# Performance work log

Hardware: AMD Instinct MI355X
Metric: run time of the kernel (lower is better)

## Reference

```python
import jax, jax.numpy as jnp
import numpy as np


def setup_inputs() -> dict:
    key = jax.random.key(0)
    k1, k2, k3, k4 = jax.random.split(key, 4)
    B, Tv, Ta, D = 8, 2048, 2048, 256
    return {
        "visual_features": jax.random.normal(k1, (B, Tv, D), dtype=jnp.float32),
        "audio_features": jax.random.normal(k2, (B, Ta, D), dtype=jnp.float32),
        "visual_weights": jax.random.uniform(k3, (D, D), dtype=jnp.float32),
        "audio_weights": jax.random.uniform(k4, (D, D), dtype=jnp.float32),
        "num_neighbors": 8,
    }


def _pairwise_l2(vm, am):
    # ||v - a|| via the expanded form to avoid the [B,Tv,Ta,D] intermediate.
    sq = (
        jnp.sum(vm * vm, -1)[:, :, None]
        + jnp.sum(am * am, -1)[:, None, :]
        - 2.0 * jnp.einsum("btd,bsd->bts", vm, am)
    )
    sq = jnp.maximum(sq, 0.0)
    # safe sqrt: subgradient 0 at 0 (matches torch.norm backward convention)
    return jnp.where(sq > 0, jnp.sqrt(jnp.where(sq > 0, sq, 1.0)), 0.0)


def reference(visual_features, audio_features, visual_weights, audio_weights, num_neighbors):
    vm = visual_features @ visual_weights  # [B,Tv,D]
    am = audio_features @ audio_weights    # [B,Ta,D]
    graph = jnp.exp(-_pairwise_l2(vm, am))  # [B,Tv,Ta]
    # topk over the visual axis (dim=1): move it last for lax.top_k
    _, idx = jax.lax.top_k(jnp.swapaxes(graph, 1, 2), num_neighbors)  # [B,Ta,k]
    idx = jnp.swapaxes(idx, 1, 2)  # [B,k,Ta]
    # broadcasted gather along axis 1: result [B,k,Ta,D]
    vn = jnp.take_along_axis(visual_features[:, :, None, :], idx[..., None], axis=1)
    an = jnp.take_along_axis(audio_features[:, :, None, :], idx[..., None], axis=1)
    # mean over dim=2 (the Ta axis of the gathered neighbors) -> [B,k,D]
    return vn.mean(axis=2), an.mean(axis=2)
```

## Files before the change

### kernel.cpp

```cpp
#include <hip/hip_runtime.h>
#include <cstddef>
#include <cstdint>

namespace {
constexpr int kB   = 8;
constexpr int kT   = 2048;
constexpr int kD   = 256;
constexpr int kK   = 8;
constexpr int kM   = kB * kT;
constexpr int kNCH = 64;
constexpr int kNC  = kB * kT;
constexpr int kColCap = 64;
constexpr int kOvCap  = 1 << 17;
constexpr int kStr = 264;
constexpr float kMinNormalF = 1.17549435e-38f;
}

typedef __attribute__((ext_vector_type(8)))  __bf16 bf16x8;
typedef __attribute__((ext_vector_type(16))) float  f32x16;

__device__ inline unsigned short f2bf_rne(float x) {
  unsigned u = __float_as_uint(x);
  unsigned r = (u + 0x7FFFu + ((u >> 16) & 1u)) >> 16;
  return (unsigned short)r;
}
__device__ inline float bf2f(unsigned short h) {
  return __uint_as_float((unsigned)h << 16);
}
union FragU { uint4 u4; bf16x8 v; };

__global__ __launch_bounds__(256) void transposeW2(const float* __restrict__ W0,
                                                   const float* __restrict__ W1,
                                                   unsigned short* __restrict__ T0,
                                                   unsigned short* __restrict__ T1) {
  const float* W = blockIdx.z ? W1 : W0;
  unsigned short* WT = blockIdx.z ? T1 : T0;
  __shared__ float tile[32][33];
  const int k0 = blockIdx.y * 32, c0 = blockIdx.x * 32;
  const int tx = threadIdx.x & 31, ty = threadIdx.x >> 5;
#pragma unroll
  for (int i = 0; i < 4; ++i)
    tile[ty + i * 8][tx] = W[(size_t)(k0 + ty + i * 8) * kD + c0 + tx];
  __syncthreads();
#pragma unroll
  for (int i = 0; i < 4; ++i)
    WT[(size_t)(c0 + ty + i * 8) * kD + k0 + tx] = f2bf_rne(tile[tx][ty + i * 8]);
}

__global__ __launch_bounds__(256) void gemm_hyb(const float* __restrict__ Xv,
                                                const float* __restrict__ Xa,
                                                const unsigned short* __restrict__ WvT,
                                                const unsigned short* __restrict__ WaT,
                                                unsigned short* __restrict__ Cv,
                                                unsigned short* __restrict__ Ca,
                                                float* __restrict__ nv,
                                                float* __restrict__ na) {
  __shared__ unsigned short S[64 * kStr];
  const int z = blockIdx.y;
  const float* X = z ? Xa : Xv;
  const unsigned short* WT = z ? WaT : WvT;
  unsigned short* Cb = z ? Ca : Cv;
  float* nrm = z ? na : nv;
  const int r0 = blockIdx.x * 64;
  const int tid = threadIdx.x;
  const int w = tid >> 6, lane = tid & 63;
  const int wt = w & 1, wc = w >> 1;
  const int half = lane >> 5, ln = lane & 31;

#pragma unroll
  for (int i = 0; i < 16; ++i) {
    const int idx = i * 256 + tid;
    const int row = idx >> 6, g = idx & 63;
    const float4 v = *reinterpret_cast<const float4*>(X + (size_t)(r0 + row) * kD + g * 4);
    ushort4 o;
    o.x = f2bf_rne(v.x); o.y = f2bf_rne(v.y); o.z = f2bf_rne(v.z); o.w = f2bf_rne(v.w);
    *reinterpret_cast<ushort4*>(S + row * kStr + g * 4) = o;
  }
  __syncthreads();
  uint4 afr[16];
#pragma unroll
  for (int kc = 0; kc < 16; ++kc)
    afr[kc] = *reinterpret_cast<const uint4*>(S + (wt * 32 + ln) * kStr + kc * 16 + half * 8);

  float ns[16];
#pragma unroll
  for (int r = 0; r < 16; ++r) ns[r] = 0.0f;

  for (int ct = 0; ct < 4; ++ct) {
    const int c0 = ct * 64;
    __syncthreads();
#pragma unroll
    for (int i = 0; i < 8; ++i) {
      const int idx = i * 256 + tid;
      const int row = idx >> 5, g = idx & 31;
      const uint4 v = *reinterpret_cast<const uint4*>(WT + (size_t)(c0 + row) * kD + g * 8);
      *reinterpret_cast<uint4*>(S + row * kStr + g * 8) = v;
    }
    __syncthreads();
    f32x16 acc;
#pragma unroll
    for (int i = 0; i < 16; ++i) acc[i] = 0.0f;
#pragma unroll
    for (int kc = 0; kc < 16; ++kc) {
      FragU fa, fb;
      fa.u4 = afr[kc];
      fb.u4 = *reinterpret_cast<const uint4*>(S + (wc * 32 + ln) * kStr + kc * 16 + half * 8);
      acc = __builtin_amdgcn_mfma_f32_32x32x16_bf16(fa.v, fb.v, acc, 0, 0, 0);
    }
    const int col = c0 + wc * 32 + ln;
#pragma unroll
    for (int r = 0; r < 16; ++r) {
      const int row = r0 + wt * 32 + (r & 3) + 8 * (r >> 2) + 4 * half;
      const unsigned short us = f2bf_rne(acc[r]);
      Cb[(size_t)row * kD + col] = us;
      const float f = bf2f(us);
      ns[r] += f * f;
    }
  }
#pragma unroll
  for (int r = 0; r < 16; ++r) {
    float v = ns[r];
#pragma unroll
    for (int off = 1; off < 32; off <<= 1) v += __shfl_xor(v, off, 64);
    if (ln == 0) {
      const int row = r0 + wt * 32 + (r & 3) + 8 * (r >> 2) + 4 * half;
      atomicAdd(nrm + row, v);
    }
  }
}

__global__ __launch_bounds__(256) void keys_hyb(const unsigned short* __restrict__ vmb,
                                                const unsigned short* __restrict__ amb,
                                                const float* __restrict__ vn2,
                                                const float* __restrict__ an2,
                                                unsigned* __restrict__ colCount,
                                                uint2* __restrict__ colRecs,
                                                unsigned* __restrict__ ovCount,
                                                uint2* __restrict__ ovRecs) {
  __shared__ unsigned short S[64 * kStr];
  const int b = blockIdx.z;
  const int t0 = blockIdx.x * 64;
  const int sr0 = blockIdx.y * 128;
  const int tid = threadIdx.x;
  const int w = tid >> 6, lane = tid & 63;
  const int wt = w & 1, wsc = w >> 1;
  const int half = lane >> 5, ln = lane & 31;

#pragma unroll
  for (int i = 0; i < 8; ++i) {
    const int idx = i * 256 + tid;
    const int row = idx >> 5, g = idx & 31;
    const uint4 v = *reinterpret_cast<const uint4*>(vmb + ((size_t)b * kT + t0 + row) * kD + g * 8);
    *reinterpret_cast<uint4*>(S + row * kStr + g * 8) = v;
  }
  __syncthreads();
  uint4 afr[16];
#pragma unroll
  for (int kc = 0; kc < 16; ++kc)
    afr[kc] = *reinterpret_cast<const uint4*>(S + (wt * 32 + ln) * kStr + kc * 16 + half * 8);

  const float* v2p = vn2 + (size_t)b * kT + t0 + wt * 32;

  for (int st = 0; st < 2; ++st) {
    const int s0 = sr0 + st * 64;
    __syncthreads();
#pragma unroll
    for (int i = 0; i < 8; ++i) {
      const int idx = i * 256 + tid;
      const int row = idx >> 5, g = idx & 31;
      const uint4 v = *reinterpret_cast<const uint4*>(amb + ((size_t)b * kT + s0 + row) * kD + g * 8);
      *reinterpret_cast<uint4*>(S + row * kStr + g * 8) = v;
    }
    __syncthreads();
    f32x16 acc;
#pragma unroll
    for (int i = 0; i < 16; ++i) acc[i] = 0.0f;
#pragma unroll
    for (int kc = 0; kc < 16; ++kc) {
      FragU fa, fb;
      fa.u4 = afr[kc];
      fb.u4 = *reinterpret_cast<const uint4*>(S + (wsc * 32 + ln) * kStr + kc * 16 + half * 8);
      acc = __builtin_amdgcn_mfma_f32_32x32x16_bf16(fa.v, fb.v, acc, 0, 0, 0);
    }
    const int s = s0 + wsc * 32 + ln;
    const float a2 = an2[(size_t)b * kT + s];
    const int c = (b << 11) | s;
#pragma unroll
    for (int g = 0; g < 4; ++g) {
      const float4 v2 = *reinterpret_cast<const float4*>(v2p + g * 8 + half * 4);
      const float v2a[4] = {v2.x, v2.y, v2.z, v2.w};
#pragma unroll
      for (int q = 0; q < 4; ++q) {
        const float raw = v2a[q] + a2 - 2.0f * acc[4 * g + q];
        if (raw < 7744.0f) {
          const float dist = sqrtf(fmaxf(raw, 0.0f));
          const float e = expf(-dist);
          if (e >= kMinNormalF) {
            const int t = t0 + wt * 32 + g * 8 + half * 4 + q;
            const unsigned slot = atomicAdd(&colCount[c], 1u);
            if (slot < (unsigned)kColCap) {
              colRecs[(size_t)c * kColCap + slot] = make_uint2(__float_as_uint(e), (unsigned)t);
            } else {
              const unsigned pos = ((unsigned)b << 22) | ((unsigned)s << 11) | (unsigned)t;
              const unsigned oi = atomicAdd(ovCount, 1u);
              if (oi < (unsigned)kOvCap) ovRecs[oi] = make_uint2(__float_as_uint(e), pos);
            }
          }
        }
      }
    }
  }
}

__global__ __launch_bounds__(256) void finalize_topk(const unsigned* __restrict__ colCount,
                                                     const uint2* __restrict__ colRecs,
                                                     const unsigned* __restrict__ ovCount,
                                                     const uint2* __restrict__ ovRecs,
                                                     int* __restrict__ idxT) {
  const int c = blockIdx.x * 256 + threadIdx.x;
  unsigned K[8];
  int T[8];
#pragma unroll
  for (int i = 0; i < 8; ++i) { K[i] = 0u; T[i] = 0x7FFFFFFF; }
  const int cnt = (int)colCount[c];
  const int m = min(cnt, kColCap);
  for (int i = 0; i < m; ++i) {
    const uint2 r = colRecs[(size_t)c * kColCap + i];
    const unsigned kx = r.x;
    const int tx = (int)r.y;
    if (kx > K[7] || (kx == K[7] && tx < T[7])) {
      K[7] = kx; T[7] = tx;
#pragma unroll
      for (int q = 7; q >= 1; --q) {
        const bool sw = (K[q] > K[q - 1]) || (K[q] == K[q - 1] && T[q] < T[q - 1]);
        if (sw) {
          const unsigned tk = K[q]; K[q] = K[q - 1]; K[q - 1] = tk;
          const int tt = T[q];      T[q] = T[q - 1]; T[q - 1] = tt;
        }
      }
    }
  }
  if (cnt > kColCap) {
    int n = (int)*ovCount;
    if (n > kOvCap) n = kOvCap;
    for (int i = 0; i < n; ++i) {
      const uint2 r = ovRecs[i];
      if ((int)(r.y >> 11) == c) {
        const unsigned kx = r.x;
        const int tx = (int)(r.y & 2047u);
        if (kx > K[7] || (kx == K[7] && tx < T[7])) {
          K[7] = kx; T[7] = tx;
#pragma unroll
          for (int q = 7; q >= 1; --q) {
            const bool sw = (K[q] > K[q - 1]) || (K[q] == K[q - 1] && T[q] < T[q - 1]);
            if (sw) {
              const unsigned tk = K[q]; K[q] = K[q - 1]; K[q - 1] = tk;
              const int tt = T[q];      T[q] = T[q - 1]; T[q - 1] = tt;
            }
          }
        }
      }
    }
  }
  int mcnt = 0;
#pragma unroll
  for (int i = 0; i < 8; ++i) if (K[i] > 0u) mcnt++;
  int outv[8];
#pragma unroll
  for (int i = 0; i < 8; ++i) outv[i] = T[i];
  int cand = 0;
  for (int r = mcnt; r < 8; ++r) {
    bool taken = true;
    while (taken) {
      taken = false;
#pragma unroll
      for (int q = 0; q < 8; ++q)
        if (q < mcnt && T[q] == cand) taken = true;
      if (taken) cand++;
    }
    outv[r] = cand++;
  }
  const int b = c >> 11, s = c & 2047;
#pragma unroll
  for (int r = 0; r < 8; ++r) idxT[((size_t)b * kK + r) * kT + s] = outv[r];
}

__global__ __launch_bounds__(256) void gather_kernel(const float* __restrict__ visual,
                                                     const float* __restrict__ audio,
                                                     const int* __restrict__ idxT,
                                                     float* __restrict__ pv,
                                                     float* __restrict__ pa) {
  const int blk = blockIdx.x;
  const int ch = blk & (kNCH - 1);
  const int bj = blk / kNCH;
  const int b = bj >> 3;
  const int d = threadIdx.x;
  const int* ip = idxT + (size_t)bj * kT + ch * (kT / kNCH);
  float accV = 0.f, accA = 0.f;
  for (int g = 0; g < kT / kNCH / 4; ++g) {
    const int4 cur = *reinterpret_cast<const int4*>(ip + g * 4);
    const int ts[4] = {cur.x, cur.y, cur.z, cur.w};
#pragma unroll
    for (int u = 0; u < 4; ++u) {
      const size_t base = ((size_t)b * kT + ts[u]) * kD + d;
      accV += visual[base];
      accA += audio[base];
    }
  }
  pv[(size_t)blk * kD + d] = accV;
  pa[(size_t)blk * kD + d] = accA;
}

__global__ __launch_bounds__(256) void reduce_kernel(const float* __restrict__ pv,
                                                     const float* __restrict__ pa,
                                                     float* __restrict__ out) {
  const int bj = blockIdx.x;
  const int d = threadIdx.x;
  float sV = 0.f, sA = 0.f;
#pragma unroll 8
  for (int ch = 0; ch < kNCH; ++ch) {
    sV += pv[((size_t)bj * kNCH + ch) * kD + d];
    sA += pa[((size_t)bj * kNCH + ch) * kD + d];
  }
  out[(size_t)bj * kD + d] = sV * (1.0f / kT);
  out[(size_t)kB * kK * kD + (size_t)bj * kD + d] = sA * (1.0f / kT);
}

extern "C" void kernel_launch(void* const* d_in, const int* in_sizes, int n_in,
                              void* d_out, int out_size, void* d_ws, size_t ws_size,
                              hipStream_t stream) {
  (void)in_sizes; (void)n_in; (void)out_size; (void)ws_size;
  const float* visual = (const float*)d_in[0];
  const float* audio  = (const float*)d_in[1];
  const float* Wv     = (const float*)d_in[2];
  const float* Wa     = (const float*)d_in[3];
  float* out = (float*)d_out;

  char* ws = (char*)d_ws;
  unsigned short* WvT = (unsigned short*)ws;
  unsigned short* WaT = WvT + (size_t)kD * kD;
  unsigned short* vmb = WaT + (size_t)kD * kD;
  unsigned short* amb = vmb + (size_t)kM * kD;
  float* vn2 = (float*)(amb + (size_t)kM * kD);
  float* an2 = vn2 + kM;
  unsigned* colCount = (unsigned*)(an2 + kM);
  unsigned* ovCount  = colCount + kNC;
  uint2* colRecs = (uint2*)(ovCount + 4);
  uint2* ovRecs  = colRecs + (size_t)kNC * kColCap;
  int* idxT = (int*)(ovRecs + kOvCap);
  float* pv = (float*)(idxT + (size_t)kB * kK * kT);
  float* pa = pv + (size_t)kB * kK * kNCH * kD;

  hipMemsetAsync(vn2, 0, (size_t)(2 * kM + kNC + 4) * sizeof(float), stream);
  transposeW2<<<dim3(kD / 32, kD / 32, 2), 256, 0, stream>>>(Wv, Wa, WvT, WaT);
  gemm_hyb<<<dim3(kM / 64, 2), 256, 0, stream>>>(visual, audio, WvT, WaT,
                                                 vmb, amb, vn2, an2);
  keys_hyb<<<dim3(kT / 64, kT / 128, kB), 256, 0, stream>>>(vmb, amb, vn2, an2,
                                                            colCount, colRecs, ovCount, ovRecs);
  finalize_topk<<<dim3(kNC / 256), 256, 0, stream>>>(colCount, colRecs, ovCount, ovRecs, idxT);
  gather_kernel<<<dim3(kB * kK * kNCH), 256, 0, stream>>>(visual, audio, idxT, pv, pa);
  reduce_kernel<<<dim3(kB * kK), 256, 0, stream>>>(pv, pa, out);
}
```

Measured before the change: 179.4 us.

## Enlarge distance-kernel tiles, split projection GEMM columns, fuse memset into prep

The pairwise-distance kernel now gives each block 128 visual rows by 256 audio rows, with each wave owning 32 visual rows and computing two 32x32 MFMA tiles per audio sub-tile. This raises reuse of the A fragments held in registers and cuts how often audio tiles are reloaded from global memory. The projection GEMM is split over two column halves to double block count. The workspace memset is folded into the weight-transpose kernel to remove a launch. The trade-offs are more accumulator registers per wave and fewer blocks in the distance kernel, while the GEMM split converts the X tile twice and adds atomic norm updates.

Measured after the change: 175.5 us. -2.2%, faster.

```diff
diff --git a/kernel.cpp b/kernel.cpp
--- a/kernel.cpp
+++ b/kernel.cpp
@@ -29,22 +29,31 @@
 }
 union FragU { uint4 u4; bf16x8 v; };
 
-__global__ __launch_bounds__(256) void transposeW2(const float* __restrict__ W0,
-                                                   const float* __restrict__ W1,
-                                                   unsigned short* __restrict__ T0,
-                                                   unsigned short* __restrict__ T1) {
-  const float* W = blockIdx.z ? W1 : W0;
-  unsigned short* WT = blockIdx.z ? T1 : T0;
-  __shared__ float tile[32][33];
-  const int k0 = blockIdx.y * 32, c0 = blockIdx.x * 32;
-  const int tx = threadIdx.x & 31, ty = threadIdx.x >> 5;
-#pragma unroll
-  for (int i = 0; i < 4; ++i)
-    tile[ty + i * 8][tx] = W[(size_t)(k0 + ty + i * 8) * kD + c0 + tx];
-  __syncthreads();
-#pragma unroll
-  for (int i = 0; i < 4; ++i)
-    WT[(size_t)(c0 + ty + i * 8) * kD + k0 + tx] = f2bf_rne(tile[tx][ty + i * 8]);
+__global__ __launch_bounds__(256) void prep(const float* __restrict__ W0,
+                                            const float* __restrict__ W1,
+                                            unsigned short* __restrict__ T0,
+                                            unsigned short* __restrict__ T1,
+                                            unsigned* __restrict__ zeroBase,
+                                            int zeroWords) {
+  const int blk = blockIdx.x;
+  if (blk < 128) {
+    const float* W = (blk & 64) ? W1 : W0;
+    unsigned short* WT = (blk & 64) ? T1 : T0;
+    const int t = blk & 63;
+    const int c0 = (t & 7) * 32, k0 = (t >> 3) * 32;
+    __shared__ float tile[32][33];
+    const int tx = threadIdx.x & 31, ty = threadIdx.x >> 5;
+#pragma unroll
+    for (int i = 0; i < 4; ++i)
+      tile[ty + i * 8][tx] = W[(size_t)(k0 + ty + i * 8) * kD + c0 + tx];
+    __syncthreads();
+#pragma unroll
+    for (int i = 0; i < 4; ++i)
+      WT[(size_t)(c0 + ty + i * 8) * kD + k0 + tx] = f2bf_rne(tile[tx][ty + i * 8]);
+  } else {
+    for (int i = (blk - 128) * 256 + threadIdx.x; i < zeroWords; i += 32 * 256)
+      zeroBase[i] = 0u;
+  }
 }
 
 __global__ __launch_bounds__(256) void gemm_hyb(const float* __restrict__ Xv,
@@ -56,12 +65,13 @@
                                                 float* __restrict__ nv,
                                                 float* __restrict__ na) {
   __shared__ unsigned short S[64 * kStr];
-  const int z = blockIdx.y;
+  const int z = blockIdx.z;
   const float* X = z ? Xa : Xv;
   const unsigned short* WT = z ? WaT : WvT;
   unsigned short* Cb = z ? Ca : Cv;
   float* nrm = z ? na : nv;
   const int r0 = blockIdx.x * 64;
+  const int cHalf = blockIdx.y;
   const int tid = threadIdx.x;
   const int w = tid >> 6, lane = tid & 63;
   const int wt = w & 1, wc = w >> 1;
@@ -86,8 +96,8 @@
 #pragma unroll
   for (int r = 0; r < 16; ++r) ns[r] = 0.0f;
 
-  for (int ct = 0; ct < 4; ++ct) {
-    const int c0 = ct * 64;
+  for (int ct = 0; ct < 2; ++ct) {
+    const int c0 = (cHalf * 2 + ct) * 64;
     __syncthreads();
 #pragma unroll
     for (int i = 0; i < 8; ++i) {
@@ -129,7 +139,7 @@
   }
 }
 
-__global__ __launch_bounds__(256) void keys_hyb(const unsigned short* __restrict__ vmb,
+__global__ __launch_bounds__(256) void keys_v12(const unsigned short* __restrict__ vmb,
                                                 const unsigned short* __restrict__ amb,
                                                 const float* __restrict__ vn2,
                                                 const float* __restrict__ an2,
@@ -139,71 +149,86 @@
                                                 uint2* __restrict__ ovRecs) {
   __shared__ unsigned short S[64 * kStr];
   const int b = blockIdx.z;
-  const int t0 = blockIdx.x * 64;
-  const int sr0 = blockIdx.y * 128;
+  const int t0 = blockIdx.x * 128;
+  const int sr0 = blockIdx.y * 256;
   const int tid = threadIdx.x;
   const int w = tid >> 6, lane = tid & 63;
-  const int wt = w & 1, wsc = w >> 1;
   const int half = lane >> 5, ln = lane & 31;
 
-#pragma unroll
-  for (int i = 0; i < 8; ++i) {
-    const int idx = i * 256 + tid;
-    const int row = idx >> 5, g = idx & 31;
-    const uint4 v = *reinterpret_cast<const uint4*>(vmb + ((size_t)b * kT + t0 + row) * kD + g * 8);
-    *reinterpret_cast<uint4*>(S + row * kStr + g * 8) = v;
-  }
-  __syncthreads();
   uint4 afr[16];
 #pragma unroll
-  for (int kc = 0; kc < 16; ++kc)
-    afr[kc] = *reinterpret_cast<const uint4*>(S + (wt * 32 + ln) * kStr + kc * 16 + half * 8);
-
-  const float* v2p = vn2 + (size_t)b * kT + t0 + wt * 32;
-
-  for (int st = 0; st < 2; ++st) {
-    const int s0 = sr0 + st * 64;
-    __syncthreads();
+  for (int h = 0; h < 2; ++h) {
 #pragma unroll
     for (int i = 0; i < 8; ++i) {
       const int idx = i * 256 + tid;
       const int row = idx >> 5, g = idx & 31;
-      const uint4 v = *reinterpret_cast<const uint4*>(amb + ((size_t)b * kT + s0 + row) * kD + g * 8);
+      const uint4 v = *reinterpret_cast<const uint4*>(
+          vmb + ((size_t)b * kT + t0 + h * 64 + row) * kD + g * 8);
       *reinterpret_cast<uint4*>(S + row * kStr + g * 8) = v;
     }
     __syncthreads();
-    f32x16 acc;
-#pragma unroll
-    for (int i = 0; i < 16; ++i) acc[i] = 0.0f;
+    if ((w >> 1) == h) {
+#pragma unroll
+      for (int kc = 0; kc < 16; ++kc)
+        afr[kc] = *reinterpret_cast<const uint4*>(S + ((w & 1) * 32 + ln) * kStr + kc * 16 + half * 8);
+    }
+    __syncthreads();
+  }
+
+  const float* v2p = vn2 + (size_t)b * kT + t0 + w * 32;
+
+  for (int st = 0; st < 4; ++st) {
+    const int s0 = sr0 + st * 64;
+    if (st) __syncthreads();
+#pragma unroll
+    for (int i = 0; i < 8; ++i) {
+      const int idx = i * 256 + tid;
+      const int row = idx >> 5, g = idx & 31;
+      const uint4 v = *reinterpret_cast<const uint4*>(
+          amb + ((size_t)b * kT + s0 + row) * kD + g * 8);
+      *reinterpret_cast<uint4*>(S + row * kStr + g * 8) = v;
+    }
+    __syncthreads();
+    f32x16 acc[2];
+#pragma unroll
+    for (int j = 0; j < 2; ++j)
+#pragma unroll
+      for (int i = 0; i < 16; ++i) acc[j][i] = 0.0f;
 #pragma unroll
     for (int kc = 0; kc < 16; ++kc) {
-      FragU fa, fb;
-      fa.u4 = afr[kc];
-      fb.u4 = *reinterpret_cast<const uint4*>(S + (wsc * 32 + ln) * kStr + kc * 16 + half * 8);
-      acc = __builtin_amdgcn_mfma_f32_32x32x16_bf16(fa.v, fb.v, acc, 0, 0, 0);
-    }
-    const int s = s0 + wsc * 32 + ln;
-    const float a2 = an2[(size_t)b * kT + s];
-    const int c = (b << 11) | s;
-#pragma unroll
-    for (int g = 0; g < 4; ++g) {
-      const float4 v2 = *reinterpret_cast<const float4*>(v2p + g * 8 + half * 4);
-      const float v2a[4] = {v2.x, v2.y, v2.z, v2.w};
-#pragma unroll
-      for (int q = 0; q < 4; ++q) {
-        const float raw = v2a[q] + a2 - 2.0f * acc[4 * g + q];
-        if (raw < 7744.0f) {
-          const float dist = sqrtf(fmaxf(raw, 0.0f));
-          const float e = expf(-dist);
-          if (e >= kMinNormalF) {
-            const int t = t0 + wt * 32 + g * 8 + half * 4 + q;
-            const unsigned slot = atomicAdd(&colCount[c], 1u);
-            if (slot < (unsigned)kColCap) {
-              colRecs[(size_t)c * kColCap + slot] = make_uint2(__float_as_uint(e), (unsigned)t);
-            } else {
-              const unsigned pos = ((unsigned)b << 22) | ((unsigned)s << 11) | (unsigned)t;
-              const unsigned oi = atomicAdd(ovCount, 1u);
-              if (oi < (unsigned)kOvCap) ovRecs[oi] = make_uint2(__float_as_uint(e), pos);
+      FragU fa; fa.u4 = afr[kc];
+#pragma unroll
+      for (int ss = 0; ss < 2; ++ss) {
+        FragU fb;
+        fb.u4 = *reinterpret_cast<const uint4*>(S + (ss * 32 + ln) * kStr + kc * 16 + half * 8);
+        acc[ss] = __builtin_amdgcn_mfma_f32_32x32x16_bf16(fa.v, fb.v, acc[ss], 0, 0, 0);
+      }
+    }
+#pragma unroll
+    for (int ss = 0; ss < 2; ++ss) {
+      const int s = s0 + ss * 32 + ln;
+      const float a2 = an2[(size_t)b * kT + s];
+      const int c = (b << 11) | s;
+#pragma unroll
+      for (int g = 0; g < 4; ++g) {
+        const float4 v2 = *reinterpret_cast<const float4*>(v2p + g * 8 + half * 4);
+        const float v2a[4] = {v2.x, v2.y, v2.z, v2.w};
+#pragma unroll
+        for (int q = 0; q < 4; ++q) {
+          const float raw = v2a[q] + a2 - 2.0f * acc[ss][4 * g + q];
+          if (raw < 7744.0f) {
+            const float dist = sqrtf(fmaxf(raw, 0.0f));
+            const float e = expf(-dist);
+            if (e >= kMinNormalF) {
+              const int t = t0 + w * 32 + g * 8 + half * 4 + q;
+              const unsigned slot = atomicAdd(&colCount[c], 1u);
+              if (slot < (unsigned)kColCap) {
+                colRecs[(size_t)c * kColCap + slot] = make_uint2(__float_as_uint(e), (unsigned)t);
+              } else {
+                const unsigned pos = ((unsigned)b << 22) | ((unsigned)s << 11) | (unsigned)t;
+                const unsigned oi = atomicAdd(ovCount, 1u);
+                if (oi < (unsigned)kOvCap) ovRecs[oi] = make_uint2(__float_as_uint(e), pos);
+              }
             }
           }
         }
@@ -345,18 +370,18 @@
   float* an2 = vn2 + kM;
   unsigned* colCount = (unsigned*)(an2 + kM);
   unsigned* ovCount  = colCount + kNC;
-  uint2* colRecs = (uint2*)(ovCount + 4);
+  uint2* colRecs = (uint2*)(ovCount + 8);
   uint2* ovRecs  = colRecs + (size_t)kNC * kColCap;
   int* idxT = (int*)(ovRecs + kOvCap);
   float* pv = (float*)(idxT + (size_t)kB * kK * kT);
   float* pa = pv + (size_t)kB * kK * kNCH * kD;
-
-  hipMemsetAsync(vn2, 0, (size_t)(2 * kM + kNC + 4) * sizeof(float), stream);
-  transposeW2<<<dim3(kD / 32, kD / 32, 2), 256, 0, stream>>>(Wv, Wa, WvT, WaT);
-  gemm_hyb<<<dim3(kM / 64, 2), 256, 0, stream>>>(visual, audio, WvT, WaT,
-                                                 vmb, amb, vn2, an2);
-  keys_hyb<<<dim3(kT / 64, kT / 128, kB), 256, 0, stream>>>(vmb, amb, vn2, an2,
-                                                            colCount, colRecs, ovCount, ovRecs);
+  const int zeroWords = 2 * kM + kNC + 8;
+
+  prep<<<dim3(160), 256, 0, stream>>>(Wv, Wa, WvT, WaT, (unsigned*)vn2, zeroWords);
+  gemm_hyb<<<dim3(kM / 64, 2, 2), 256, 0, stream>>>(visual, audio, WvT, WaT,
+                                                    vmb, amb, vn2, an2);
+  keys_v12<<<dim3(kT / 128, kT / 256, kB), 256, 0, stream>>>(vmb, amb, vn2, an2,
+                                                             colCount, colRecs, ovCount, ovRecs);
   finalize_topk<<<dim3(kNC / 256), 256, 0, stream>>>(colCount, colRecs, ovCount, ovRecs, idxT);
   gather_kernel<<<dim3(kB * kK * kNCH), 256, 0, stream>>>(visual, audio, idxT, pv, pa);
   reduce_kernel<<<dim3(kB * kK), 256, 0, stream>>>(pv, pa, out);
```
